# Kernel optimization log

Hardware: AMD Instinct MI355X
Metric: run time of the kernel (lower is better)

The kernel has to match this reference:

```python
import jax, jax.numpy as jnp
import numpy as np

B, S, D, H = 4, 2048, 768, 12
DK = D // H


def setup_inputs() -> dict:
    key = jax.random.key(0)
    ks = jax.random.split(key, 13)
    s = 1.0 / np.sqrt(D)
    inp = {
        "q": jax.random.normal(ks[0], (B, S, D), jnp.float32),
        "k": jax.random.normal(ks[1], (B, S, D), jnp.float32),
        "v": jax.random.normal(ks[2], (B, S, D), jnp.float32),
        "mask": jax.random.randint(ks[3], (B, S), 0, 2, jnp.int32),
        "Wq": jax.random.normal(ks[4], (D, D), jnp.float32) * s,
        "bq": jnp.zeros((D,), jnp.float32),
        "Wk": jax.random.normal(ks[5], (D, D), jnp.float32) * s,
        "bk": jnp.zeros((D,), jnp.float32),
        "Wv": jax.random.normal(ks[6], (D, D), jnp.float32) * s,
        "bv": jnp.zeros((D,), jnp.float32),
        "Wo": jax.random.normal(ks[7], (D, D), jnp.float32) * s,
        "bo": jnp.zeros((D,), jnp.float32),
    }
    return inp


def reference(q, k, v, mask, Wq, bq, Wk, bk, Wv, bv, Wo, bo):
    b, s, d = q.shape
    # projections (torch Linear: x @ W.T + b), split into heads: [b, h, s, dk]
    Q = (q @ Wq.T + bq).reshape(b, s, H, DK).transpose(0, 2, 1, 3)
    K = (k @ Wk.T + bk).reshape(b, s, H, DK).transpose(0, 2, 1, 3)
    V = (v @ Wv.T + bv).reshape(b, s, H, DK).transpose(0, 2, 1, 3)
    scores = jnp.einsum("bhqd,bhkd->bhqk", Q, K) / jnp.sqrt(jnp.float32(DK))
    # mask [b,s] -> [b,1,s,1]: masks whole query rows (faithful to source)
    scores = jnp.where(mask[:, None, :, None] == 0, jnp.float32(-1e9), scores)
    attn = jax.nn.softmax(scores, axis=-1)  # dropout is identity at inference
    out = jnp.einsum("bhqk,bhkd->bhqd", attn, V)
    concat = out.transpose(0, 2, 1, 3).reshape(b, s, d)
    return concat @ Wo.T + bo
```

## Files before the change

kernel.cpp:

```cpp
#include <hip/hip_runtime.h>

typedef _Float16 f16;
typedef f16 f16x4 __attribute__((ext_vector_type(4)));
typedef f16 f16x8 __attribute__((ext_vector_type(8)));
typedef float f32x4 __attribute__((ext_vector_type(4)));

#define B_ 4
#define S_ 2048
#define D_ 768
#define H_ 12
#define DK_ 64

__device__ __forceinline__ void dma16(const f16* g, f16* l) {
    __builtin_amdgcn_global_load_lds(
        (__attribute__((address_space(1))) void*)(uintptr_t)g,
        (__attribute__((address_space(3))) void*)l, 16, 0, 0);
}

struct Cvt7 { const float* s[7]; f16* d[7]; int n[7]; };

__global__ __launch_bounds__(256) void cvt7_kernel(Cvt7 a)
{
    const int z = blockIdx.y;
    int i = (blockIdx.x * 256 + threadIdx.x) * 8;
    if (i >= a.n[z]) return;
    const float* __restrict__ s = a.s[z];
    float4 x = *(const float4*)(s + i);
    float4 y = *(const float4*)(s + i + 4);
    f16x8 h = {(f16)x.x, (f16)x.y, (f16)x.z, (f16)x.w,
               (f16)y.x, (f16)y.y, (f16)y.z, (f16)y.w};
    *(f16x8*)(a.d[z] + i) = h;
}

struct GemmArgs { const f16* A; const f16* W; const float* bias; float scale; void* C; int mode; };
struct GemmArgs3 { GemmArgs g[3]; };

__global__ __launch_bounds__(256, 4) void gemm_k(GemmArgs3 args)
{
    const int z = blockIdx.z;
    const f16* __restrict__ A = args.g[z].A;
    const f16* __restrict__ W = args.g[z].W;
    const float* __restrict__ bias = args.g[z].bias;
    const float scale = args.g[z].scale;
    const int mode = args.g[z].mode;

    __shared__ __align__(16) f16 As[128 * 64];
    __shared__ __align__(16) f16 Bs[128 * 64];

    const int tid = threadIdx.x, lane = tid & 63, w = tid >> 6;
    const int l15 = lane & 15, lg = lane >> 4;
    const int wm = (w >> 1) * 64, wn = (w & 1) * 64;
    const int m0 = blockIdx.y * 128, n0 = blockIdx.x * 128;

    const int lrow8 = lane >> 3;
    const int lchk8 = (lane & 7) ^ lrow8;
    const f16* gA = A + (size_t)(m0 + w * 32 + lrow8) * D_ + lchk8 * 8;
    const f16* gB = W + (size_t)(n0 + w * 32 + lrow8) * D_ + lchk8 * 8;

    f32x4 acc[4][4] = {};

    for (int kt = 0; kt < D_; kt += 64) {
        __syncthreads();
#pragma unroll
        for (int c = 0; c < 4; ++c) {
            dma16(gA + (size_t)(c * 8) * D_ + kt, &As[(w * 4 + c) * 512]);
            dma16(gB + (size_t)(c * 8) * D_ + kt, &Bs[(w * 4 + c) * 512]);
        }
        __syncthreads();
#pragma unroll
        for (int kk = 0; kk < 2; ++kk) {
            const int chk = ((kk * 4 + lg) ^ (l15 & 7)) * 8;
            f16x8 af[4], bf[4];
#pragma unroll
            for (int i = 0; i < 4; ++i)
                af[i] = *(const f16x8*)&As[(wm + i * 16 + l15) * 64 + chk];
#pragma unroll
            for (int j = 0; j < 4; ++j)
                bf[j] = *(const f16x8*)&Bs[(wn + j * 16 + l15) * 64 + chk];
#pragma unroll
            for (int i = 0; i < 4; ++i)
#pragma unroll
                for (int j = 0; j < 4; ++j)
                    acc[i][j] = __builtin_amdgcn_mfma_f32_16x16x32_f16(
                        af[i], bf[j], acc[i][j], 0, 0, 0);
        }
    }

    if (mode == 1) {
#pragma unroll
        for (int j = 0; j < 4; ++j) {
            int col = n0 + wn + j * 16 + l15;
            float bb = bias[col];
#pragma unroll
            for (int i = 0; i < 4; ++i) {
                int row = m0 + wm + i * 16 + lg * 4;
                int bI = row >> 11, sl = row & (S_ - 1);
                f16x4 o = {(f16)(acc[i][j][0] + bb), (f16)(acc[i][j][1] + bb),
                           (f16)(acc[i][j][2] + bb), (f16)(acc[i][j][3] + bb)};
                *(f16x4*)&((f16*)args.g[z].C)[((size_t)bI * D_ + col) * S_ + sl] = o;
            }
        }
    } else if (mode == 0) {
#pragma unroll
        for (int j = 0; j < 4; ++j) {
            int col = n0 + wn + j * 16 + l15;
            float bb = bias[col];
#pragma unroll
            for (int i = 0; i < 4; ++i) {
                int row = m0 + wm + i * 16 + lg * 4;
#pragma unroll
                for (int r = 0; r < 4; ++r)
                    ((f16*)args.g[z].C)[(size_t)(row + r) * D_ + col] =
                        (f16)((acc[i][j][r] + bb) * scale);
            }
        }
    } else {
#pragma unroll
        for (int j = 0; j < 4; ++j) {
            int col = n0 + wn + j * 16 + l15;
            float bb = bias[col];
#pragma unroll
            for (int i = 0; i < 4; ++i) {
                int row = m0 + wm + i * 16 + lg * 4;
#pragma unroll
                for (int r = 0; r < 4; ++r)
                    ((float*)args.g[z].C)[(size_t)(row + r) * D_ + col] =
                        acc[i][j][r] + bb;
            }
        }
    }
}

__global__ __launch_bounds__(256, 3) void attn_k(
    const f16* __restrict__ Qh, const f16* __restrict__ Kh,
    const f16* __restrict__ VhT, const int* __restrict__ mask,
    f16* __restrict__ O)
{
    __shared__ __align__(16) f16 Ks[128 * 64];
    __shared__ __align__(16) f16 Vt[64 * 128];
    const int tid = threadIdx.x, lane = tid & 63, w = tid >> 6;
    const int l15 = lane & 15, lg = lane >> 4;

    const int bid = blockIdx.x;
    const int g8 = bid & 7, j5 = bid >> 3;
    const int head_lin = g8 * 6 + (j5 >> 4);
    const int qt = j5 & 15;
    const int b = head_lin / H_, h = head_lin % H_;
    const int q0 = qt * 128;
    const int rowbase = b * S_;
    const int col0 = h * DK_;

    const int lrow8 = lane >> 3;
    const int lchk8 = (lane & 7) ^ lrow8;

    {
        const f16* Qbase = Qh + (size_t)(rowbase + q0 + w * 32 + lrow8) * D_ + col0 + lchk8 * 8;
#pragma unroll
        for (int c = 0; c < 4; ++c)
            dma16(Qbase + (size_t)(c * 8) * D_, &Ks[(w * 4 + c) * 512]);
    }
    __syncthreads();
    f16x8 qf[2][2];
#pragma unroll
    for (int ns = 0; ns < 2; ++ns) {
        float mf = (mask[rowbase + q0 + w * 32 + ns * 16 + l15] != 0) ? 1.0f : 0.0f;
#pragma unroll
        for (int kk = 0; kk < 2; ++kk) {
            f16x8 t = *(const f16x8*)&Ks[(w * 32 + ns * 16 + l15) * 64 +
                                         (((kk * 4 + lg) ^ (l15 & 7)) * 8)];
#pragma unroll
            for (int e = 0; e < 8; ++e) t[e] = (f16)((float)t[e] * mf);
            qf[ns][kk] = t;
        }
    }

    const f16* Kbase = Kh + (size_t)rowbase * D_ + col0;
    const f16* Vbase = VhT + ((size_t)b * D_ + col0) * S_;
    const int vrow4 = lane >> 4;
    const int vchk = lane & 15;

    float lrun[2] = {0.f, 0.f};
    f32x4 acc[4][2] = {};

    for (int t = 0; t < S_ / 128; ++t) {
        const int k0 = t * 128;
        __syncthreads();
#pragma unroll
        for (int c = 0; c < 4; ++c)
            dma16(Kbase + (size_t)(k0 + w * 32 + c * 8 + lrow8) * D_ + lchk8 * 8,
                  &Ks[(w * 4 + c) * 512]);
#pragma unroll
        for (int c = 0; c < 4; ++c) {
            int o = w * 4 + c;
            int drow = o * 4 + vrow4;
            int gchk = vchk ^ (drow & 15);
            dma16(Vbase + (size_t)drow * S_ + k0 + gchk * 8, &Vt[o * 512]);
        }
        __syncthreads();

        f32x4 sf[8][2] = {};
#pragma unroll
        for (int kk = 0; kk < 2; ++kk) {
            const int chk = ((kk * 4 + lg) ^ (l15 & 7)) * 8;
#pragma unroll
            for (int ms = 0; ms < 8; ++ms) {
                f16x8 kf = *(const f16x8*)&Ks[(ms * 16 + l15) * 64 + chk];
                sf[ms][0] = __builtin_amdgcn_mfma_f32_16x16x32_f16(
                    kf, qf[0][kk], sf[ms][0], 0, 0, 0);
                sf[ms][1] = __builtin_amdgcn_mfma_f32_16x16x32_f16(
                    kf, qf[1][kk], sf[ms][1], 0, 0, 0);
            }
        }

        f16x4 pf[8][2];
#pragma unroll
        for (int ns = 0; ns < 2; ++ns) {
            float rs = 0.f;
#pragma unroll
            for (int ms = 0; ms < 8; ++ms) {
                float p0 = __builtin_exp2f(sf[ms][ns][0]);
                float p1 = __builtin_exp2f(sf[ms][ns][1]);
                float p2 = __builtin_exp2f(sf[ms][ns][2]);
                float p3 = __builtin_exp2f(sf[ms][ns][3]);
                rs += (p0 + p1) + (p2 + p3);
                pf[ms][ns] = {(f16)p0, (f16)p1, (f16)p2, (f16)p3};
            }
            rs += __shfl_xor(rs, 16, 64);
            rs += __shfl_xor(rs, 32, 64);
            lrun[ns] += rs;
        }

#pragma unroll
        for (int c = 0; c < 8; ++c) {
            const int pchk = (((c * 2 + (lg >> 1)) ^ l15) * 8) + (lg & 1) * 4;
#pragma unroll
            for (int i = 0; i < 4; ++i) {
                f16x4 vf = *(const f16x4*)&Vt[(i * 16 + l15) * 128 + pchk];
                acc[i][0] = __builtin_amdgcn_mfma_f32_16x16x16f16(
                    vf, pf[c][0], acc[i][0], 0, 0, 0);
                acc[i][1] = __builtin_amdgcn_mfma_f32_16x16x16f16(
                    vf, pf[c][1], acc[i][1], 0, 0, 0);
            }
        }
    }

#pragma unroll
    for (int ns = 0; ns < 2; ++ns) {
        float inv = 1.0f / lrun[ns];
        size_t qrow = (size_t)(rowbase + q0 + w * 32 + ns * 16 + l15);
#pragma unroll
        for (int i = 0; i < 4; ++i) {
            f32x4 o = acc[i][ns] * inv;
            f16x4 ho = {(f16)o[0], (f16)o[1], (f16)o[2], (f16)o[3]};
            *(f16x4*)&O[qrow * D_ + col0 + i * 16 + lg * 4] = ho;
        }
    }
}

extern "C" void kernel_launch(void* const* d_in, const int* in_sizes, int n_in,
                              void* d_out, int out_size, void* d_ws, size_t ws_size,
                              hipStream_t stream)
{
    const float* q    = (const float*)d_in[0];
    const float* k    = (const float*)d_in[1];
    const float* v    = (const float*)d_in[2];
    const int*   mask = (const int*)d_in[3];
    const float* Wq   = (const float*)d_in[4];
    const float* bq   = (const float*)d_in[5];
    const float* Wk   = (const float*)d_in[6];
    const float* bk   = (const float*)d_in[7];
    const float* Wv   = (const float*)d_in[8];
    const float* bv   = (const float*)d_in[9];
    const float* Wo   = (const float*)d_in[10];
    const float* bo   = (const float*)d_in[11];

    const size_t nQKV = (size_t)B_ * S_ * D_;
    const size_t nW   = (size_t)D_ * D_;

    f16* qh  = (f16*)d_ws;
    f16* kh  = qh + nQKV;
    f16* vh  = kh + nQKV;
    f16* Wqh = vh + nQKV;
    f16* Wkh = Wqh + nW;
    f16* Wvh = Wkh + nW;
    f16* Woh = Wvh + nW;
    f16* Qp  = Woh + nW;
    f16* Kp  = Qp + nQKV;
    f16* VpT = Kp + nQKV;
    f16* Cp  = VpT + nQKV;

    Cvt7 cv = {{q, k, v, Wq, Wk, Wv, Wo},
               {qh, kh, vh, Wqh, Wkh, Wvh, Woh},
               {(int)nQKV, (int)nQKV, (int)nQKV, (int)nW, (int)nW, (int)nW, (int)nW}};
    cvt7_kernel<<<dim3((int)(nQKV / 8 / 256), 7), 256, 0, stream>>>(cv);

    GemmArgs3 g1 = {{{qh, Wqh, bq, 1.44269504f / 8.0f, (void*)Qp, 0},
                     {kh, Wkh, bk, 1.0f, (void*)Kp, 0},
                     {vh, Wvh, bv, 1.0f, (void*)VpT, 1}}};
    gemm_k<<<dim3(6, 64, 3), 256, 0, stream>>>(g1);

    attn_k<<<dim3(768), 256, 0, stream>>>(Qp, Kp, VpT, mask, Cp);

    GemmArgs3 g2 = {{{Cp, Woh, bo, 1.0f, d_out, 2},
                     {Cp, Woh, bo, 1.0f, d_out, 2},
                     {Cp, Woh, bo, 1.0f, d_out, 2}}};
    gemm_k<<<dim3(6, 64, 1), 256, 0, stream>>>(g2);
}
```

Baseline: 296.6 us.

## Drop LDS staging, read operands directly from global, fuse fp32 input conversion into GEMM

Removes the fp32-to-fp16 conversion pass over q/k/v and instead converts on the fly inside the projection GEMM. Both the GEMM and the attention kernel stop staging tiles in shared memory and load MFMA operands straight from global memory, so the barriers disappear but each wave re-fetches data without cross-wave LDS reuse. The softmax row-sum is now computed with an extra MFMA against a ones vector instead of shuffles. This trades LDS traffic and synchronisation for more global/L2 load traffic and possibly poorly coalesced strided loads.

Result: slower. 609.7 us (+105.5%).

```diff
diff --git a/kernel.cpp b/kernel.cpp
--- a/kernel.cpp
+++ b/kernel.cpp
@@ -11,19 +11,12 @@
 #define H_ 12
 #define DK_ 64
 
-__device__ __forceinline__ void dma16(const f16* g, f16* l) {
-    __builtin_amdgcn_global_load_lds(
-        (__attribute__((address_space(1))) void*)(uintptr_t)g,
-        (__attribute__((address_space(3))) void*)l, 16, 0, 0);
-}
-
-struct Cvt7 { const float* s[7]; f16* d[7]; int n[7]; };
-
-__global__ __launch_bounds__(256) void cvt7_kernel(Cvt7 a)
+struct Cvt4 { const float* s[4]; f16* d[4]; };
+
+__global__ __launch_bounds__(256) void cvt4_kernel(Cvt4 a)
 {
     const int z = blockIdx.y;
     int i = (blockIdx.x * 256 + threadIdx.x) * 8;
-    if (i >= a.n[z]) return;
     const float* __restrict__ s = a.s[z];
     float4 x = *(const float4*)(s + i);
     float4 y = *(const float4*)(s + i + 4);
@@ -32,58 +25,57 @@
     *(f16x8*)(a.d[z] + i) = h;
 }
 
-struct GemmArgs { const f16* A; const f16* W; const float* bias; float scale; void* C; int mode; };
+struct GemmArgs { const void* A; const f16* W; const float* bias; float scale; void* C; int mode; };
 struct GemmArgs3 { GemmArgs g[3]; };
 
-__global__ __launch_bounds__(256, 4) void gemm_k(GemmArgs3 args)
+template<bool AF32>
+__global__ __launch_bounds__(256, 3) void gemm_k(GemmArgs3 args)
 {
     const int z = blockIdx.z;
-    const f16* __restrict__ A = args.g[z].A;
     const f16* __restrict__ W = args.g[z].W;
     const float* __restrict__ bias = args.g[z].bias;
     const float scale = args.g[z].scale;
     const int mode = args.g[z].mode;
 
-    __shared__ __align__(16) f16 As[128 * 64];
-    __shared__ __align__(16) f16 Bs[128 * 64];
-
     const int tid = threadIdx.x, lane = tid & 63, w = tid >> 6;
     const int l15 = lane & 15, lg = lane >> 4;
     const int wm = (w >> 1) * 64, wn = (w & 1) * 64;
     const int m0 = blockIdx.y * 128, n0 = blockIdx.x * 128;
 
-    const int lrow8 = lane >> 3;
-    const int lchk8 = (lane & 7) ^ lrow8;
-    const f16* gA = A + (size_t)(m0 + w * 32 + lrow8) * D_ + lchk8 * 8;
-    const f16* gB = W + (size_t)(n0 + w * 32 + lrow8) * D_ + lchk8 * 8;
+    const float* aP32[4];
+    const f16*   aP16[4];
+    const f16*   bP[4];
+#pragma unroll
+    for (int i = 0; i < 4; ++i) {
+        size_t row = (size_t)(m0 + wm + i * 16 + l15);
+        if (AF32) aP32[i] = (const float*)args.g[z].A + row * D_ + lg * 8;
+        else      aP16[i] = (const f16*)args.g[z].A + row * D_ + lg * 8;
+        bP[i] = W + (size_t)(n0 + wn + i * 16 + l15) * D_ + lg * 8;
+    }
 
     f32x4 acc[4][4] = {};
 
-    for (int kt = 0; kt < D_; kt += 64) {
-        __syncthreads();
-#pragma unroll
-        for (int c = 0; c < 4; ++c) {
-            dma16(gA + (size_t)(c * 8) * D_ + kt, &As[(w * 4 + c) * 512]);
-            dma16(gB + (size_t)(c * 8) * D_ + kt, &Bs[(w * 4 + c) * 512]);
-        }
-        __syncthreads();
-#pragma unroll
-        for (int kk = 0; kk < 2; ++kk) {
-            const int chk = ((kk * 4 + lg) ^ (l15 & 7)) * 8;
-            f16x8 af[4], bf[4];
-#pragma unroll
-            for (int i = 0; i < 4; ++i)
-                af[i] = *(const f16x8*)&As[(wm + i * 16 + l15) * 64 + chk];
+#pragma unroll 2
+    for (int kt = 0; kt < D_; kt += 32) {
+        f16x8 af[4], bf[4];
+#pragma unroll
+        for (int i = 0; i < 4; ++i) {
+            if (AF32) {
+                float4 x = *(const float4*)(aP32[i] + kt);
+                float4 y = *(const float4*)(aP32[i] + kt + 4);
+                af[i] = f16x8{(f16)x.x, (f16)x.y, (f16)x.z, (f16)x.w,
+                              (f16)y.x, (f16)y.y, (f16)y.z, (f16)y.w};
+            } else {
+                af[i] = *(const f16x8*)(aP16[i] + kt);
+            }
+            bf[i] = *(const f16x8*)(bP[i] + kt);
+        }
+#pragma unroll
+        for (int i = 0; i < 4; ++i)
 #pragma unroll
             for (int j = 0; j < 4; ++j)
-                bf[j] = *(const f16x8*)&Bs[(wn + j * 16 + l15) * 64 + chk];
-#pragma unroll
-            for (int i = 0; i < 4; ++i)
-#pragma unroll
-                for (int j = 0; j < 4; ++j)
-                    acc[i][j] = __builtin_amdgcn_mfma_f32_16x16x32_f16(
-                        af[i], bf[j], acc[i][j], 0, 0, 0);
-        }
+                acc[i][j] = __builtin_amdgcn_mfma_f32_16x16x32_f16(
+                    af[i], bf[j], acc[i][j], 0, 0, 0);
     }
 
     if (mode == 1) {
@@ -136,8 +128,6 @@
     const f16* __restrict__ VhT, const int* __restrict__ mask,
     f16* __restrict__ O)
 {
-    __shared__ __align__(16) f16 Ks[128 * 64];
-    __shared__ __align__(16) f16 Vt[64 * 128];
     const int tid = threadIdx.x, lane = tid & 63, w = tid >> 6;
     const int l15 = lane & 15, lg = lane >> 4;
 
@@ -150,103 +140,71 @@
     const int rowbase = b * S_;
     const int col0 = h * DK_;
 
-    const int lrow8 = lane >> 3;
-    const int lchk8 = (lane & 7) ^ lrow8;
-
-    {
-        const f16* Qbase = Qh + (size_t)(rowbase + q0 + w * 32 + lrow8) * D_ + col0 + lchk8 * 8;
-#pragma unroll
-        for (int c = 0; c < 4; ++c)
-            dma16(Qbase + (size_t)(c * 8) * D_, &Ks[(w * 4 + c) * 512]);
-    }
-    __syncthreads();
     f16x8 qf[2][2];
 #pragma unroll
     for (int ns = 0; ns < 2; ++ns) {
+        const f16* qp = Qh + (size_t)(rowbase + q0 + w * 32 + ns * 16 + l15) * D_ + col0;
         float mf = (mask[rowbase + q0 + w * 32 + ns * 16 + l15] != 0) ? 1.0f : 0.0f;
 #pragma unroll
         for (int kk = 0; kk < 2; ++kk) {
-            f16x8 t = *(const f16x8*)&Ks[(w * 32 + ns * 16 + l15) * 64 +
-                                         (((kk * 4 + lg) ^ (l15 & 7)) * 8)];
+            f16x8 t = *(const f16x8*)(qp + kk * 32 + lg * 8);
 #pragma unroll
             for (int e = 0; e < 8; ++e) t[e] = (f16)((float)t[e] * mf);
             qf[ns][kk] = t;
         }
     }
 
-    const f16* Kbase = Kh + (size_t)rowbase * D_ + col0;
+    const f16* Kbase = Kh + (size_t)rowbase * D_ + col0 + lg * 8;
     const f16* Vbase = VhT + ((size_t)b * D_ + col0) * S_;
-    const int vrow4 = lane >> 4;
-    const int vchk = lane & 15;
-
-    float lrun[2] = {0.f, 0.f};
+
+    const f16x4 kones = {(f16)1.f, (f16)1.f, (f16)1.f, (f16)1.f};
     f32x4 acc[4][2] = {};
+    f32x4 acc_l[2] = {};
 
     for (int t = 0; t < S_ / 128; ++t) {
         const int k0 = t * 128;
-        __syncthreads();
-#pragma unroll
-        for (int c = 0; c < 4; ++c)
-            dma16(Kbase + (size_t)(k0 + w * 32 + c * 8 + lrow8) * D_ + lchk8 * 8,
-                  &Ks[(w * 4 + c) * 512]);
-#pragma unroll
-        for (int c = 0; c < 4; ++c) {
-            int o = w * 4 + c;
-            int drow = o * 4 + vrow4;
-            int gchk = vchk ^ (drow & 15);
-            dma16(Vbase + (size_t)drow * S_ + k0 + gchk * 8, &Vt[o * 512]);
-        }
-        __syncthreads();
-
-        f32x4 sf[8][2] = {};
-#pragma unroll
-        for (int kk = 0; kk < 2; ++kk) {
-            const int chk = ((kk * 4 + lg) ^ (l15 & 7)) * 8;
-#pragma unroll
-            for (int ms = 0; ms < 8; ++ms) {
-                f16x8 kf = *(const f16x8*)&Ks[(ms * 16 + l15) * 64 + chk];
-                sf[ms][0] = __builtin_amdgcn_mfma_f32_16x16x32_f16(
-                    kf, qf[0][kk], sf[ms][0], 0, 0, 0);
-                sf[ms][1] = __builtin_amdgcn_mfma_f32_16x16x32_f16(
-                    kf, qf[1][kk], sf[ms][1], 0, 0, 0);
-            }
-        }
 
         f16x4 pf[8][2];
 #pragma unroll
-        for (int ns = 0; ns < 2; ++ns) {
-            float rs = 0.f;
-#pragma unroll
-            for (int ms = 0; ms < 8; ++ms) {
-                float p0 = __builtin_exp2f(sf[ms][ns][0]);
-                float p1 = __builtin_exp2f(sf[ms][ns][1]);
-                float p2 = __builtin_exp2f(sf[ms][ns][2]);
-                float p3 = __builtin_exp2f(sf[ms][ns][3]);
-                rs += (p0 + p1) + (p2 + p3);
-                pf[ms][ns] = {(f16)p0, (f16)p1, (f16)p2, (f16)p3};
-            }
-            rs += __shfl_xor(rs, 16, 64);
-            rs += __shfl_xor(rs, 32, 64);
-            lrun[ns] += rs;
+        for (int ms = 0; ms < 8; ++ms) {
+            const f16* kp = Kbase + (size_t)(k0 + ms * 16 + l15) * D_;
+            f16x8 kf0 = *(const f16x8*)(kp);
+            f16x8 kf1 = *(const f16x8*)(kp + 32);
+            f32x4 s0 = {}, s1 = {};
+            s0 = __builtin_amdgcn_mfma_f32_16x16x32_f16(kf0, qf[0][0], s0, 0, 0, 0);
+            s1 = __builtin_amdgcn_mfma_f32_16x16x32_f16(kf0, qf[1][0], s1, 0, 0, 0);
+            s0 = __builtin_amdgcn_mfma_f32_16x16x32_f16(kf1, qf[0][1], s0, 0, 0, 0);
+            s1 = __builtin_amdgcn_mfma_f32_16x16x32_f16(kf1, qf[1][1], s1, 0, 0, 0);
+            pf[ms][0] = {(f16)__builtin_exp2f(s0[0]), (f16)__builtin_exp2f(s0[1]),
+                         (f16)__builtin_exp2f(s0[2]), (f16)__builtin_exp2f(s0[3])};
+            pf[ms][1] = {(f16)__builtin_exp2f(s1[0]), (f16)__builtin_exp2f(s1[1]),
+                         (f16)__builtin_exp2f(s1[2]), (f16)__builtin_exp2f(s1[3])};
         }
 
 #pragma unroll
         for (int c = 0; c < 8; ++c) {
-            const int pchk = (((c * 2 + (lg >> 1)) ^ l15) * 8) + (lg & 1) * 4;
-#pragma unroll
-            for (int i = 0; i < 4; ++i) {
-                f16x4 vf = *(const f16x4*)&Vt[(i * 16 + l15) * 128 + pchk];
+            f16x4 vf[4];
+#pragma unroll
+            for (int i = 0; i < 4; ++i)
+                vf[i] = *(const f16x4*)(Vbase + (size_t)(i * 16 + l15) * S_ +
+                                        k0 + c * 16 + lg * 4);
+#pragma unroll
+            for (int i = 0; i < 4; ++i) {
                 acc[i][0] = __builtin_amdgcn_mfma_f32_16x16x16f16(
-                    vf, pf[c][0], acc[i][0], 0, 0, 0);
+                    vf[i], pf[c][0], acc[i][0], 0, 0, 0);
                 acc[i][1] = __builtin_amdgcn_mfma_f32_16x16x16f16(
-                    vf, pf[c][1], acc[i][1], 0, 0, 0);
-            }
+                    vf[i], pf[c][1], acc[i][1], 0, 0, 0);
+            }
+            acc_l[0] = __builtin_amdgcn_mfma_f32_16x16x16f16(
+                kones, pf[c][0], acc_l[0], 0, 0, 0);
+            acc_l[1] = __builtin_amdgcn_mfma_f32_16x16x16f16(
+                kones, pf[c][1], acc_l[1], 0, 0, 0);
         }
     }
 
 #pragma unroll
     for (int ns = 0; ns < 2; ++ns) {
-        float inv = 1.0f / lrun[ns];
+        float inv = 1.0f / acc_l[ns][0];
         size_t qrow = (size_t)(rowbase + q0 + w * 32 + ns * 16 + l15);
 #pragma unroll
         for (int i = 0; i < 4; ++i) {
@@ -277,10 +235,7 @@
     const size_t nQKV = (size_t)B_ * S_ * D_;
     const size_t nW   = (size_t)D_ * D_;
 
-    f16* qh  = (f16*)d_ws;
-    f16* kh  = qh + nQKV;
-    f16* vh  = kh + nQKV;
-    f16* Wqh = vh + nQKV;
+    f16* Wqh = (f16*)d_ws;
     f16* Wkh = Wqh + nW;
     f16* Wvh = Wkh + nW;
     f16* Woh = Wvh + nW;
@@ -289,20 +244,18 @@
     f16* VpT = Kp + nQKV;
     f16* Cp  = VpT + nQKV;
 
-    Cvt7 cv = {{q, k, v, Wq, Wk, Wv, Wo},
-               {qh, kh, vh, Wqh, Wkh, Wvh, Woh},
-               {(int)nQKV, (int)nQKV, (int)nQKV, (int)nW, (int)nW, (int)nW, (int)nW}};
-    cvt7_kernel<<<dim3((int)(nQKV / 8 / 256), 7), 256, 0, stream>>>(cv);
-
-    GemmArgs3 g1 = {{{qh, Wqh, bq, 1.44269504f / 8.0f, (void*)Qp, 0},
-                     {kh, Wkh, bk, 1.0f, (void*)Kp, 0},
-                     {vh, Wvh, bv, 1.0f, (void*)VpT, 1}}};
-    gemm_k<<<dim3(6, 64, 3), 256, 0, stream>>>(g1);
+    Cvt4 cv = {{Wq, Wk, Wv, Wo}, {Wqh, Wkh, Wvh, Woh}};
+    cvt4_kernel<<<dim3((int)(nW / 8 / 256), 4), 256, 0, stream>>>(cv);
+
+    GemmArgs3 g1 = {{{q, Wqh, bq, 1.44269504f / 8.0f, (void*)Qp, 0},
+                     {k, Wkh, bk, 1.0f, (void*)Kp, 0},
+                     {v, Wvh, bv, 1.0f, (void*)VpT, 1}}};
+    gemm_k<true><<<dim3(6, 64, 3), 256, 0, stream>>>(g1);
 
     attn_k<<<dim3(768), 256, 0, stream>>>(Qp, Kp, VpT, mask, Cp);
 
     GemmArgs3 g2 = {{{Cp, Woh, bo, 1.0f, d_out, 2},
                      {Cp, Woh, bo, 1.0f, d_out, 2},
                      {Cp, Woh, bo, 1.0f, d_out, 2}}};
-    gemm_k<<<dim3(6, 64, 1), 256, 0, stream>>>(g2);
-}
+    gemm_k<false><<<dim3(6, 64, 1), 256, 0, stream>>>(g2);
+}
```
